# Optimization experiments

Hardware: AMD Instinct MI355X
Metric: run time of the kernel (lower is better)

## Reference

```python
import jax, jax.numpy as jnp
import numpy as np

B, S, D, E, HD, F, L, CYCLES = 2, 1024, 1000, 20, 50, 2048, 14, 3


def setup_inputs() -> dict:
    key = jax.random.key(0)
    k = jax.random.split(key, 8)
    sc = 0.02
    return {
        "x": jax.random.normal(k[0], (B, S, D), jnp.float32),
        "expert_w": jax.random.normal(k[1], (L, E, D, 3 * HD), jnp.float32) * sc,
        "expert_b": jnp.zeros((L, E, 3 * HD), jnp.float32),
        "router_w": jax.random.normal(k[2], (L, D, E), jnp.float32) * sc,
        "router_b": jnp.zeros((L, E), jnp.float32),
        "out_w": jax.random.normal(k[3], (L, D, D), jnp.float32) * sc,
        "out_b": jnp.zeros((L, D), jnp.float32),
        "ln1_g": jnp.ones((L, D), jnp.float32),
        "ln1_b": jnp.zeros((L, D), jnp.float32),
        "ff_w1": jax.random.normal(k[4], (L, D, F), jnp.float32) * sc,
        "ff_b1": jnp.zeros((L, F), jnp.float32),
        "ff_w2": jax.random.normal(k[5], (L, F, D), jnp.float32) * sc,
        "ff_b2": jnp.zeros((L, D), jnp.float32),
        "ln2_g": jnp.ones((L, D), jnp.float32),
        "ln2_b": jnp.zeros((L, D), jnp.float32),
    }


def _layer_norm(x, g, b):
    m = jnp.mean(x, -1, keepdims=True)
    v = jnp.mean((x - m) ** 2, -1, keepdims=True)
    return (x - m) * jax.lax.rsqrt(v + 1e-5) * g + b


def _moe_attn(x, ew, eb, rw, rb, ow, ob):
    # x: [b, s, d]; ew: [E, d, 3*HD]; routing softmax over experts
    b_, s_, d_ = x.shape
    routing = jax.nn.softmax(x @ rw + rb, axis=-1)           # [b, s, E]
    qkv = jnp.einsum('bsd,edh->besh', x, ew) + eb[None, :, None, :]
    q, k, v = jnp.split(qkv, 3, axis=-1)                     # each [b, E, s, HD]
    scores = jnp.einsum('besh,beth->best', q, k) * (HD ** -0.5)
    attn = jax.nn.softmax(scores, axis=-1)
    out = jnp.einsum('best,beth->besh', attn, v)             # [b, E, s, HD]
    out = out * jnp.transpose(routing, (0, 2, 1))[..., None]
    # disjoint head slices -> reshape is exactly the torch slice-add combine
    out = jnp.transpose(out, (0, 2, 1, 3)).reshape(b_, s_, d_)
    return out @ ow + ob


def _block(x, i, p):
    a = _moe_attn(x, p['expert_w'][i], p['expert_b'][i], p['router_w'][i],
                  p['router_b'][i], p['out_w'][i], p['out_b'][i])
    x = _layer_norm(x + a, p['ln1_g'][i], p['ln1_b'][i])
    h = jax.nn.gelu(x @ p['ff_w1'][i] + p['ff_b1'][i], approximate=False)
    f = h @ p['ff_w2'][i] + p['ff_b2'][i]
    return _layer_norm(x + f, p['ln2_g'][i], p['ln2_b'][i])


def _slam(x, p):
    s = x.shape[1]
    x = _block(x, 0, p)
    bounds = [(0, min(int(s * 0.45), s)),
              (max(int(s * 0.25), 0), min(int(s * 0.65), s)),
              (max(int(s * 0.45), 0), min(int(s * 0.85), s)),
              (max(int(s * 0.65), 0), s)]
    wrap = max(min(int(s * 0.05), s // 10), 1) if s > 20 else 0
    counts = np.zeros(s, np.float32)
    for st, en in bounds:
        counts[st:en] += 1.0
    if wrap:
        counts[:wrap] += 1.0
    counts = jnp.asarray(np.maximum(counts, 1.0))[None, :, None]
    for c in range(CYCLES):
        x_new = jnp.zeros_like(x)
        for j, (st, en) in enumerate(bounds):
            li = 1 + 4 * c + j
            if j == 3 and wrap:
                seg = jnp.concatenate([x[:, st:s], x[:, :wrap]], axis=1)
                out = _block(seg, li, p)
                x_new = x_new.at[:, st:s].add(out[:, :s - st])
                x_new = x_new.at[:, :wrap].add(out[:, s - st:])
            else:
                out = _block(x[:, st:en], li, p)
                x_new = x_new.at[:, st:en].add(out)
        x = x_new / counts
    return _block(x, L - 1, p)


def reference(x, expert_w, expert_b, router_w, router_b, out_w, out_b,
              ln1_g, ln1_b, ff_w1, ff_b1, ff_w2, ff_b2, ln2_g, ln2_b):
    p = dict(expert_w=expert_w, expert_b=expert_b, router_w=router_w,
             router_b=router_b, out_w=out_w, out_b=out_b, ln1_g=ln1_g,
             ln1_b=ln1_b, ff_w1=ff_w1, ff_b1=ff_b1, ff_w2=ff_w2,
             ff_b2=ff_b2, ln2_g=ln2_g, ln2_b=ln2_b)
    return _slam(x, p)
```

## Files before the change

### kernel.cpp

```cpp
#include <hip/hip_runtime.h>
#include <math.h>

namespace {

constexpr int kB  = 2;
constexpr int kS  = 1024;
constexpr int kD  = 1000;
constexpr int kE  = 20;
constexpr int kHD = 50;
constexpr int kF  = 2048;
constexpr int kQKV = 3 * kHD;

__global__ __launch_bounds__(256) void zero_kernel(float* __restrict__ p, int n) {
    int i = blockIdx.x * 256 + threadIdx.x;
    if (i < n) p[i] = 0.0f;
}

__global__ __launch_bounds__(256) void gelu_kernel(float* __restrict__ p, int n) {
    int i = blockIdx.x * 256 + threadIdx.x;
    if (i < n) {
        float x = p[i];
        p[i] = 0.5f * x * (1.0f + erff(x * 0.70710678118654752440f));
    }
}

__global__ __launch_bounds__(256) void gather_kernel(const float* __restrict__ src,
                                                     float* __restrict__ dst,
                                                     int st, int sseg) {
    int i = blockIdx.x * 256 + threadIdx.x;
    int tot = kB * sseg * kD;
    if (i >= tot) return;
    int d  = i % kD;
    int tr = i / kD;
    int r  = tr % sseg;
    int b  = tr / sseg;
    int srow = st + r;
    if (srow >= kS) srow -= kS;
    dst[i] = src[(b * kS + srow) * kD + d];
}

__global__ __launch_bounds__(256) void scatter_add_kernel(const float* __restrict__ src,
                                                          float* __restrict__ dst,
                                                          int st, int sseg) {
    int i = blockIdx.x * 256 + threadIdx.x;
    int tot = kB * sseg * kD;
    if (i >= tot) return;
    int d  = i % kD;
    int tr = i / kD;
    int r  = tr % sseg;
    int b  = tr / sseg;
    int drow = st + r;
    if (drow >= kS) drow -= kS;
    dst[(b * kS + drow) * kD + d] += src[i];
}

__global__ __launch_bounds__(256) void finalize_kernel(const float* __restrict__ xn,
                                                       float* __restrict__ cur) {
    int i = blockIdx.x * 256 + threadIdx.x;
    const int tot = kB * kS * kD;
    if (i >= tot) return;
    int r = (i / kD) % kS;
    float cnt = 0.0f;
    cnt += (r < 460) ? 1.0f : 0.0f;
    cnt += (r >= 256 && r < 665) ? 1.0f : 0.0f;
    cnt += (r >= 460 && r < 870) ? 1.0f : 0.0f;
    cnt += (r >= 665) ? 1.0f : 0.0f;
    cnt += (r < 51) ? 1.0f : 0.0f;
    cnt = fmaxf(cnt, 1.0f);
    cur[i] = xn[i] / cnt;
}

template<int BM, int BN, int TM, int TN>
__global__ __launch_bounds__(256) void gemm_tile(
    const float* __restrict__ A, const float* __restrict__ W,
    const float* __restrict__ bias, float* __restrict__ C,
    int M, int N, int K,
    long long strideW, long long strideC, long long strideBias)
{
    constexpr int BK = 16;
    constexpr int TX = BN / TN;
    constexpr int TY = BM / TM;
    static_assert(TX * TY == 256, "block must be 256 threads");
    static_assert(TM % 4 == 0 && TN % 4 == 0, "vector frags");

    W    += (long long)blockIdx.z * strideW;
    C    += (long long)blockIdx.z * strideC;
    bias += (long long)blockIdx.z * strideBias;

    __shared__ float As[BK][BM + 4];
    __shared__ float Bs[BK][BN];

    const int tid  = threadIdx.x;
    const int tx   = tid % TX;
    const int ty   = tid / TX;
    const int row0 = blockIdx.y * BM;
    const int col0 = blockIdx.x * BN;

    const bool nvec = (N % 4) == 0;
    const bool kvec = (K % 4) == 0;

    float acc[TM][TN] = {};

    const int nk = (K + BK - 1) / BK;
    for (int t = 0; t < nk; t++) {
        const int k0 = t * BK;

        #pragma unroll
        for (int i = 0; i < BM / 64; i++) {
            int f  = tid + i * 256;
            int r  = f >> 2;
            int cv = f & 3;
            int gr = row0 + r;
            int gc = k0 + cv * 4;
            float4 av = make_float4(0.f, 0.f, 0.f, 0.f);
            if (gr < M) {
                if (kvec && gc + 3 < K) {
                    av = *reinterpret_cast<const float4*>(A + (long long)gr * K + gc);
                } else {
                    float t0 = (gc + 0 < K) ? A[(long long)gr * K + gc + 0] : 0.f;
                    float t1 = (gc + 1 < K) ? A[(long long)gr * K + gc + 1] : 0.f;
                    float t2 = (gc + 2 < K) ? A[(long long)gr * K + gc + 2] : 0.f;
                    float t3 = (gc + 3 < K) ? A[(long long)gr * K + gc + 3] : 0.f;
                    av = make_float4(t0, t1, t2, t3);
                }
            }
            As[cv * 4 + 0][r] = av.x;
            As[cv * 4 + 1][r] = av.y;
            As[cv * 4 + 2][r] = av.z;
            As[cv * 4 + 3][r] = av.w;
        }

        if (nvec) {
            #pragma unroll
            for (int i = 0; i < BN / 64; i++) {
                int f  = tid + i * 256;
                int r  = f / (BN / 4);
                int cv = f % (BN / 4);
                int gr = k0 + r;
                int gc = col0 + cv * 4;
                float4 bv = make_float4(0.f, 0.f, 0.f, 0.f);
                if (gr < K) {
                    if (gc + 3 < N) {
                        bv = *reinterpret_cast<const float4*>(W + (long long)gr * N + gc);
                    } else {
                        float t0 = (gc + 0 < N) ? W[(long long)gr * N + gc + 0] : 0.f;
                        float t1 = (gc + 1 < N) ? W[(long long)gr * N + gc + 1] : 0.f;
                        float t2 = (gc + 2 < N) ? W[(long long)gr * N + gc + 2] : 0.f;
                        float t3 = (gc + 3 < N) ? W[(long long)gr * N + gc + 3] : 0.f;
                        bv = make_float4(t0, t1, t2, t3);
                    }
                }
                *reinterpret_cast<float4*>(&Bs[r][cv * 4]) = bv;
            }
        } else {
            for (int idx = tid; idx < BK * BN; idx += 256) {
                int r = idx / BN, c = idx % BN;
                int gr = k0 + r, gc = col0 + c;
                Bs[r][c] = (gr < K && gc < N) ? W[(long long)gr * N + gc] : 0.f;
            }
        }
        __syncthreads();

        #pragma unroll
        for (int kk = 0; kk < BK; kk++) {
            float a[TM], b[TN];
            #pragma unroll
            for (int i = 0; i < TM; i += 4) {
                float4 v = *reinterpret_cast<const float4*>(&As[kk][ty * TM + i]);
                a[i] = v.x; a[i + 1] = v.y; a[i + 2] = v.z; a[i + 3] = v.w;
            }
            #pragma unroll
            for (int j = 0; j < TN; j += 4) {
                float4 v = *reinterpret_cast<const float4*>(&Bs[kk][tx * TN + j]);
                b[j] = v.x; b[j + 1] = v.y; b[j + 2] = v.z; b[j + 3] = v.w;
            }
            #pragma unroll
            for (int i = 0; i < TM; i++)
                #pragma unroll
                for (int j = 0; j < TN; j++)
                    acc[i][j] = fmaf(a[i], b[j], acc[i][j]);
        }
        __syncthreads();
    }

    #pragma unroll
    for (int i = 0; i < TM; i++) {
        int gr = row0 + ty * TM + i;
        if (gr >= M) continue;
        if (nvec) {
            #pragma unroll
            for (int j = 0; j < TN; j += 4) {
                int gc = col0 + tx * TN + j;
                if (gc + 3 < N) {
                    float4 bv = *reinterpret_cast<const float4*>(bias + gc);
                    float4 o  = make_float4(acc[i][j + 0] + bv.x,
                                            acc[i][j + 1] + bv.y,
                                            acc[i][j + 2] + bv.z,
                                            acc[i][j + 3] + bv.w);
                    *reinterpret_cast<float4*>(C + (long long)gr * N + gc) = o;
                } else {
                    for (int jj = 0; jj < 4; jj++) {
                        int g = gc + jj;
                        if (g < N) C[(long long)gr * N + g] = acc[i][j + jj] + bias[g];
                    }
                }
            }
        } else {
            #pragma unroll
            for (int j = 0; j < TN; j++) {
                int gc = col0 + tx * TN + j;
                if (gc < N) C[(long long)gr * N + gc] = acc[i][j] + bias[gc];
            }
        }
    }
}

template<int BM, int BN, int TM, int TN>
inline void launch_gemm(const float* A, const float* W, const float* bias, float* C,
                        int M, int N, int K, int Z,
                        long long sW, long long sC, long long sB, hipStream_t stream)
{
    dim3 grid((N + BN - 1) / BN, (M + BM - 1) / BM, Z);
    gemm_tile<BM, BN, TM, TN><<<grid, 256, 0, stream>>>(A, W, bias, C, M, N, K, sW, sC, sB);
}

__global__ __launch_bounds__(256) void routing_kernel(
    const float* __restrict__ X, const float* __restrict__ RW,
    const float* __restrict__ RB, float* __restrict__ R, int T)
{
    int wave = (blockIdx.x * 256 + threadIdx.x) / 64;
    int lane = threadIdx.x & 63;
    if (wave >= T) return;
    const float* x = X + (long long)wave * kD;

    float xr[16];
    #pragma unroll
    for (int i = 0; i < 16; i++) {
        int d = lane + 64 * i;
        xr[i] = (d < kD) ? x[d] : 0.0f;
    }
    float r[kE];
    #pragma unroll
    for (int e = 0; e < kE; e++) {
        float acc = 0.0f;
        #pragma unroll
        for (int i = 0; i < 16; i++) {
            int d = lane + 64 * i;
            if (d < kD) acc = fmaf(xr[i], RW[d * kE + e], acc);
        }
        #pragma unroll
        for (int off = 32; off > 0; off >>= 1) acc += __shfl_xor(acc, off, 64);
        r[e] = acc + RB[e];
    }
    float m = r[0];
    #pragma unroll
    for (int e = 1; e < kE; e++) m = fmaxf(m, r[e]);
    float sum = 0.0f;
    #pragma unroll
    for (int e = 0; e < kE; e++) { r[e] = expf(r[e] - m); sum += r[e]; }
    float inv = 1.0f / sum;
    float mine = 0.0f;
    #pragma unroll
    for (int e = 0; e < kE; e++) if (lane == e) mine = r[e] * inv;
    if (lane < kE) R[(long long)wave * kE + lane] = mine;
}

__global__ __launch_bounds__(256) void attn_kernel(
    const float* __restrict__ QKV, const float* __restrict__ R,
    float* __restrict__ O, int s)
{
    const int q0 = blockIdx.x * 64;
    const int e  = blockIdx.y;
    const int b  = blockIdx.z;
    const int T  = kB * s;
    const float* base = QKV + ((long long)e * T + (long long)b * s) * kQKV;

    __shared__ float Qs[64][51];
    __shared__ float Ks[64][51];
    __shared__ float Vs[64][51];
    __shared__ float Sb[64][65];
    __shared__ float mrow[64], lrow[64], arow[64];

    const int tid = threadIdx.x;
    const int tx = tid & 15, ty = tid >> 4;

    for (int idx = tid; idx < 64 * kHD; idx += 256) {
        int r = idx / kHD, h = idx % kHD;
        int q = q0 + r;
        Qs[r][h] = (q < s) ? base[(long long)q * kQKV + h] : 0.0f;
    }
    if (tid < 64) { mrow[tid] = -1e30f; lrow[tid] = 0.0f; }

    float o[4][4] = {};

    for (int k0 = 0; k0 < s; k0 += 64) {
        const int kn = min(64, s - k0);
        __syncthreads();
        for (int idx = tid; idx < 64 * kHD; idx += 256) {
            int r = idx / kHD, h = idx % kHD;
            const float* row = base + (long long)(k0 + r) * kQKV;
            bool ok = (r < kn);
            Ks[r][h] = ok ? row[kHD + h] : 0.0f;
            Vs[r][h] = ok ? row[2 * kHD + h] : 0.0f;
        }
        __syncthreads();

        float sacc[4][4] = {};
        for (int kk = 0; kk < kHD; kk++) {
            float a[4], bb[4];
            #pragma unroll
            for (int i = 0; i < 4; i++) a[i] = Qs[ty * 4 + i][kk];
            #pragma unroll
            for (int j = 0; j < 4; j++) bb[j] = Ks[tx * 4 + j][kk];
            #pragma unroll
            for (int i = 0; i < 4; i++)
                #pragma unroll
                for (int j = 0; j < 4; j++)
                    sacc[i][j] = fmaf(a[i], bb[j], sacc[i][j]);
        }
        #pragma unroll
        for (int i = 0; i < 4; i++)
            #pragma unroll
            for (int j = 0; j < 4; j++)
                Sb[ty * 4 + i][tx * 4 + j] = sacc[i][j] * 0.14142135623730950488f;
        __syncthreads();

        if (tid < 64) {
            float m_old = mrow[tid];
            float tmax = -1e30f;
            for (int j = 0; j < kn; j++) tmax = fmaxf(tmax, Sb[tid][j]);
            float m_new = fmaxf(m_old, tmax);
            float alpha = __expf(m_old - m_new);
            float rs = 0.0f;
            for (int j = 0; j < 64; j++) {
                float p = (j < kn) ? __expf(Sb[tid][j] - m_new) : 0.0f;
                Sb[tid][j] = p;
                rs += p;
            }
            mrow[tid] = m_new;
            lrow[tid] = lrow[tid] * alpha + rs;
            arow[tid] = alpha;
        }
        __syncthreads();

        float al[4];
        #pragma unroll
        for (int i = 0; i < 4; i++) al[i] = arow[ty * 4 + i];
        #pragma unroll
        for (int i = 0; i < 4; i++)
            #pragma unroll
            for (int j = 0; j < 4; j++)
                o[i][j] *= al[i];
        for (int j = 0; j < 64; j++) {
            float p[4], v[4];
            #pragma unroll
            for (int i = 0; i < 4; i++) p[i] = Sb[ty * 4 + i][j];
            #pragma unroll
            for (int c = 0; c < 4; c++) v[c] = Vs[j][tx * 4 + c];
            #pragma unroll
            for (int i = 0; i < 4; i++)
                #pragma unroll
                for (int c = 0; c < 4; c++)
                    o[i][c] = fmaf(p[i], v[c], o[i][c]);
        }
    }

    __syncthreads();
    #pragma unroll
    for (int i = 0; i < 4; i++)
        #pragma unroll
        for (int j = 0; j < 4; j++) {
            int h = tx * 4 + j;
            if (h < kHD) Sb[ty * 4 + i][h] = o[i][j];
        }
    __syncthreads();
    for (int idx = tid; idx < 64 * kHD; idx += 256) {
        int r = idx / kHD, h = idx % kHD;
        int q = q0 + r;
        if (q < s) {
            long long t = (long long)b * s + q;
            float scale = R[t * kE + e] / lrow[r];
            O[t * kD + e * kHD + h] = Sb[r][h] * scale;
        }
    }
}

__global__ __launch_bounds__(256) void ln_kernel(
    const float* __restrict__ Xres, const float* __restrict__ A,
    const float* __restrict__ G, const float* __restrict__ Bb,
    float* __restrict__ Y)
{
    const int t = blockIdx.x;
    const float* x = Xres + (long long)t * kD;
    const float* a = A + (long long)t * kD;
    __shared__ float buf[kD];
    __shared__ float red[4];
    const int tid = threadIdx.x;

    float lsum = 0.0f;
    for (int d = tid; d < kD; d += 256) {
        float v = x[d] + a[d];
        buf[d] = v;
        lsum += v;
    }
    #pragma unroll
    for (int off = 32; off > 0; off >>= 1) lsum += __shfl_xor(lsum, off, 64);
    if ((tid & 63) == 0) red[tid >> 6] = lsum;
    __syncthreads();
    float mean = (red[0] + red[1] + red[2] + red[3]) * (1.0f / kD);

    float lv = 0.0f;
    for (int d = tid; d < kD; d += 256) {
        float u = buf[d] - mean;
        lv = fmaf(u, u, lv);
    }
    #pragma unroll
    for (int off = 32; off > 0; off >>= 1) lv += __shfl_xor(lv, off, 64);
    __syncthreads();
    if ((tid & 63) == 0) red[tid >> 6] = lv;
    __syncthreads();
    float var = (red[0] + red[1] + red[2] + red[3]) * (1.0f / kD);
    float inv = rsqrtf(var + 1e-5f);

    for (int d = tid; d < kD; d += 256)
        Y[(long long)t * kD + d] = (buf[d] - mean) * inv * G[d] + Bb[d];
}

struct Params {
    const float *expert_w, *expert_b, *router_w, *router_b, *out_w, *out_b;
    const float *ln1_g, *ln1_b, *ff_w1, *ff_b1, *ff_w2, *ff_b2, *ln2_g, *ln2_b;
};

void run_block(const float* xin, float* xout, int s, int li, const Params& P,
               float* routing, float* qkv, float* attn_comb, float* a_out,
               float* y1, float* h, float* f, hipStream_t stream)
{
    const int T = kB * s;

    routing_kernel<<<(T + 3) / 4, 256, 0, stream>>>(
        xin, P.router_w + (long long)li * kD * kE, P.router_b + li * kE, routing, T);

    launch_gemm<128, 64, 8, 4>(
        xin, P.expert_w + (long long)li * kE * kD * kQKV,
        P.expert_b + (long long)li * kE * kQKV, qkv,
        T, kQKV, kD, kE,
        (long long)kD * kQKV, (long long)T * kQKV, (long long)kQKV, stream);

    {
        dim3 grid((s + 63) / 64, kE, kB);
        attn_kernel<<<grid, 256, 0, stream>>>(qkv, routing, attn_comb, s);
    }

    if (T >= 1536)
        launch_gemm<128, 64, 8, 4>(attn_comb, P.out_w + (long long)li * kD * kD,
                                   P.out_b + li * kD, a_out, T, kD, kD, 1, 0, 0, 0, stream);
    else
        launch_gemm<64, 64, 4, 4>(attn_comb, P.out_w + (long long)li * kD * kD,
                                  P.out_b + li * kD, a_out, T, kD, kD, 1, 0, 0, 0, stream);

    ln_kernel<<<T, 256, 0, stream>>>(xin, a_out, P.ln1_g + li * kD, P.ln1_b + li * kD, y1);

    if (T >= 1536)
        launch_gemm<128, 128, 8, 8>(y1, P.ff_w1 + (long long)li * kD * kF,
                                    P.ff_b1 + li * kF, h, T, kF, kD, 1, 0, 0, 0, stream);
    else
        launch_gemm<128, 64, 8, 4>(y1, P.ff_w1 + (long long)li * kD * kF,
                                   P.ff_b1 + li * kF, h, T, kF, kD, 1, 0, 0, 0, stream);

    gelu_kernel<<<(T * kF + 255) / 256, 256, 0, stream>>>(h, T * kF);

    if (T >= 1536)
        launch_gemm<128, 64, 8, 4>(h, P.ff_w2 + (long long)li * kF * kD,
                                   P.ff_b2 + li * kD, f, T, kD, kF, 1, 0, 0, 0, stream);
    else
        launch_gemm<64, 64, 4, 4>(h, P.ff_w2 + (long long)li * kF * kD,
                                  P.ff_b2 + li * kD, f, T, kD, kF, 1, 0, 0, 0, stream);

    ln_kernel<<<T, 256, 0, stream>>>(y1, f, P.ln2_g + li * kD, P.ln2_b + li * kD, xout);
}

}

extern "C" void kernel_launch(void* const* d_in, const int* in_sizes, int n_in,
                              void* d_out, int out_size, void* d_ws, size_t ws_size,
                              hipStream_t stream)
{
    const float* x = (const float*)d_in[0];
    Params P;
    P.expert_w = (const float*)d_in[1];
    P.expert_b = (const float*)d_in[2];
    P.router_w = (const float*)d_in[3];
    P.router_b = (const float*)d_in[4];
    P.out_w    = (const float*)d_in[5];
    P.out_b    = (const float*)d_in[6];
    P.ln1_g    = (const float*)d_in[7];
    P.ln1_b    = (const float*)d_in[8];
    P.ff_w1    = (const float*)d_in[9];
    P.ff_b1    = (const float*)d_in[10];
    P.ff_w2    = (const float*)d_in[11];
    P.ff_b2    = (const float*)d_in[12];
    P.ln2_g    = (const float*)d_in[13];
    P.ln2_b    = (const float*)d_in[14];

    const int TD = kB * kS * kD;
    float* ws = (float*)d_ws;
    float* cur       = ws;  ws += TD;
    float* xnew      = ws;  ws += TD;
    float* seg       = ws;  ws += TD;
    float* routing   = ws;  ws += kB * kS * kE;
    float* qkv       = ws;  ws += kE * kB * kS * kQKV;
    float* attn_comb = ws;  ws += TD;
    float* a_out     = ws;  ws += TD;
    float* y1        = ws;  ws += TD;
    float* h         = ws;  ws += kB * kS * kF;
    float* f         = ws;  ws += TD;
    float* bout      = (float*)d_out;

    run_block(x, cur, kS, 0, P, routing, qkv, attn_comb, a_out, y1, h, f, stream);

    const int st_arr[4]  = {0, 256, 460, 665};
    const int len_arr[4] = {460, 409, 410, 410};

    for (int c = 0; c < 3; c++) {
        zero_kernel<<<(TD + 255) / 256, 256, 0, stream>>>(xnew, TD);
        for (int j = 0; j < 4; j++) {
            const int st = st_arr[j], sl = len_arr[j];
            const int li = 1 + 4 * c + j;
            const int n = kB * sl * kD;
            gather_kernel<<<(n + 255) / 256, 256, 0, stream>>>(cur, seg, st, sl);
            run_block(seg, bout, sl, li, P, routing, qkv, attn_comb, a_out, y1, h, f, stream);
            scatter_add_kernel<<<(n + 255) / 256, 256, 0, stream>>>(bout, xnew, st, sl);
        }
        finalize_kernel<<<(TD + 255) / 256, 256, 0, stream>>>(xnew, cur);
    }

    run_block(cur, (float*)d_out, kS, 13, P, routing, qkv, attn_comb, a_out, y1, h, f, stream);
}
```

Measured before the change: 12.96 ms.

## Add split-K atomic GEMM, fused expert QKV GEMM, and register-softmax attention

Introduces a split-K GEMM path that pre-fills the output with bias and accumulates partial K-chunks with atomicAdd, picking the split from the grid size so small segment GEMMs fill the GPU. The per-expert batched QKV GEMM becomes one wide GEMM over E*3*HD columns with an index map into the per-expert layout. The attention kernel moves the online softmax into registers using wave shuffles, transposes Q/K in shared memory for float4 reads, and reuses the K buffer for the probabilities. The atomics add traffic and make the sums nondeterministic, and the mapped weight loads in the QKV GEMM are scalar rather than vectorised.

```diff
diff --git a/kernel.cpp b/kernel.cpp
--- a/kernel.cpp
+++ b/kernel.cpp
@@ -22,6 +22,13 @@
         float x = p[i];
         p[i] = 0.5f * x * (1.0f + erff(x * 0.70710678118654752440f));
     }
+}
+
+__global__ __launch_bounds__(256) void init_bias_kernel(float* __restrict__ C,
+                                                        const float* __restrict__ bias,
+                                                        long long total, int N) {
+    long long i = (long long)blockIdx.x * 256 + threadIdx.x;
+    if (i < total) C[i] = bias[(int)(i % N)];
 }
 
 __global__ __launch_bounds__(256) void gather_kernel(const float* __restrict__ src,
@@ -70,11 +77,11 @@
     cur[i] = xn[i] / cnt;
 }
 
-template<int BM, int BN, int TM, int TN>
+template<int BM, int BN, int TM, int TN, int NMAP, bool ATOMIC>
 __global__ __launch_bounds__(256) void gemm_tile(
     const float* __restrict__ A, const float* __restrict__ W,
     const float* __restrict__ bias, float* __restrict__ C,
-    int M, int N, int K,
+    int M, int N, int K, int kchunk,
     long long strideW, long long strideC, long long strideBias)
 {
     constexpr int BK = 16;
@@ -83,12 +90,18 @@
     static_assert(TX * TY == 256, "block must be 256 threads");
     static_assert(TM % 4 == 0 && TN % 4 == 0, "vector frags");
 
-    W    += (long long)blockIdx.z * strideW;
-    C    += (long long)blockIdx.z * strideC;
-    bias += (long long)blockIdx.z * strideBias;
-
-    __shared__ float As[BK][BM + 4];
-    __shared__ float Bs[BK][BN];
+    int kbeg = 0, kend = K;
+    if (ATOMIC) {
+        kbeg = blockIdx.z * kchunk;
+        kend = min(K, kbeg + kchunk);
+    } else {
+        W    += (long long)blockIdx.z * strideW;
+        C    += (long long)blockIdx.z * strideC;
+        bias += (long long)blockIdx.z * strideBias;
+    }
+
+    __shared__ __align__(16) float As[BK][BM + 4];
+    __shared__ __align__(16) float Bs[BK][BN];
 
     const int tid  = threadIdx.x;
     const int tx   = tid % TX;
@@ -96,15 +109,9 @@
     const int row0 = blockIdx.y * BM;
     const int col0 = blockIdx.x * BN;
 
-    const bool nvec = (N % 4) == 0;
-    const bool kvec = (K % 4) == 0;
-
     float acc[TM][TN] = {};
 
-    const int nk = (K + BK - 1) / BK;
-    for (int t = 0; t < nk; t++) {
-        const int k0 = t * BK;
-
+    for (int k0 = kbeg; k0 < kend; k0 += BK) {
         #pragma unroll
         for (int i = 0; i < BM / 64; i++) {
             int f  = tid + i * 256;
@@ -114,13 +121,13 @@
             int gc = k0 + cv * 4;
             float4 av = make_float4(0.f, 0.f, 0.f, 0.f);
             if (gr < M) {
-                if (kvec && gc + 3 < K) {
+                if (gc + 3 < kend) {
                     av = *reinterpret_cast<const float4*>(A + (long long)gr * K + gc);
                 } else {
-                    float t0 = (gc + 0 < K) ? A[(long long)gr * K + gc + 0] : 0.f;
-                    float t1 = (gc + 1 < K) ? A[(long long)gr * K + gc + 1] : 0.f;
-                    float t2 = (gc + 2 < K) ? A[(long long)gr * K + gc + 2] : 0.f;
-                    float t3 = (gc + 3 < K) ? A[(long long)gr * K + gc + 3] : 0.f;
+                    float t0 = (gc + 0 < kend) ? A[(long long)gr * K + gc + 0] : 0.f;
+                    float t1 = (gc + 1 < kend) ? A[(long long)gr * K + gc + 1] : 0.f;
+                    float t2 = (gc + 2 < kend) ? A[(long long)gr * K + gc + 2] : 0.f;
+                    float t3 = (gc + 3 < kend) ? A[(long long)gr * K + gc + 3] : 0.f;
                     av = make_float4(t0, t1, t2, t3);
                 }
             }
@@ -130,7 +137,21 @@
             As[cv * 4 + 3][r] = av.w;
         }
 
-        if (nvec) {
+        if (NMAP > 0) {
+            #pragma unroll
+            for (int it = 0; it < (BK * BN) / 256; it++) {
+                int idx = tid + it * 256;
+                int r = idx / BN, c = idx % BN;
+                int gr = k0 + r, gc = col0 + c;
+                float v = 0.f;
+                if (gr < kend && gc < N) {
+                    int e = gc / NMAP;
+                    int n = gc - e * NMAP;
+                    v = W[(long long)e * K * NMAP + (long long)gr * NMAP + n];
+                }
+                Bs[r][c] = v;
+            }
+        } else {
             #pragma unroll
             for (int i = 0; i < BN / 64; i++) {
                 int f  = tid + i * 256;
@@ -139,7 +160,7 @@
                 int gr = k0 + r;
                 int gc = col0 + cv * 4;
                 float4 bv = make_float4(0.f, 0.f, 0.f, 0.f);
-                if (gr < K) {
+                if (gr < kend) {
                     if (gc + 3 < N) {
                         bv = *reinterpret_cast<const float4*>(W + (long long)gr * N + gc);
                     } else {
@@ -152,12 +173,6 @@
                 }
                 *reinterpret_cast<float4*>(&Bs[r][cv * 4]) = bv;
             }
-        } else {
-            for (int idx = tid; idx < BK * BN; idx += 256) {
-                int r = idx / BN, c = idx % BN;
-                int gr = k0 + r, gc = col0 + c;
-                Bs[r][c] = (gr < K && gc < N) ? W[(long long)gr * N + gc] : 0.f;
-            }
         }
         __syncthreads();
 
@@ -187,7 +202,24 @@
     for (int i = 0; i < TM; i++) {
         int gr = row0 + ty * TM + i;
         if (gr >= M) continue;
-        if (nvec) {
+        if (ATOMIC) {
+            #pragma unroll
+            for (int j = 0; j < TN; j++) {
+                int gc = col0 + tx * TN + j;
+                if (gc < N) atomicAdd(&C[(long long)gr * N + gc], acc[i][j]);
+            }
+        } else if (NMAP > 0) {
+            #pragma unroll
+            for (int j = 0; j < TN; j++) {
+                int gc = col0 + tx * TN + j;
+                if (gc < N) {
+                    int e = gc / NMAP;
+                    int n = gc - e * NMAP;
+                    C[(long long)e * M * NMAP + (long long)gr * NMAP + n] =
+                        acc[i][j] + bias[gc];
+                }
+            }
+        } else {
             #pragma unroll
             for (int j = 0; j < TN; j += 4) {
                 int gc = col0 + tx * TN + j;
@@ -205,23 +237,38 @@
                     }
                 }
             }
-        } else {
-            #pragma unroll
-            for (int j = 0; j < TN; j++) {
-                int gc = col0 + tx * TN + j;
-                if (gc < N) C[(long long)gr * N + gc] = acc[i][j] + bias[gc];
-            }
-        }
-    }
-}
-
-template<int BM, int BN, int TM, int TN>
-inline void launch_gemm(const float* A, const float* W, const float* bias, float* C,
-                        int M, int N, int K, int Z,
-                        long long sW, long long sC, long long sB, hipStream_t stream)
+        }
+    }
+}
+
+inline int pick_split(int gx, int gy, int K) {
+    int blocks = gx * gy;
+    int S = (512 + blocks - 1) / blocks;
+    if (S < 1) S = 1;
+    if (S > 4) S = 4;
+    while (S > 1 && (K + S - 1) / S < 64) S--;
+    return S;
+}
+
+inline void gemm_auto(const float* A, const float* W, const float* bias, float* C,
+                      int M, int N, int K, hipStream_t stream)
 {
-    dim3 grid((N + BN - 1) / BN, (M + BM - 1) / BM, Z);
-    gemm_tile<BM, BN, TM, TN><<<grid, 256, 0, stream>>>(A, W, bias, C, M, N, K, sW, sC, sB);
+    constexpr int BM = 128, BN = 64, TM = 8, TN = 4;
+    int gx = (N + BN - 1) / BN, gy = (M + BM - 1) / BM;
+    int S = pick_split(gx, gy, K);
+    if (S == 1) {
+        dim3 grid(gx, gy, 1);
+        gemm_tile<BM, BN, TM, TN, 0, false><<<grid, 256, 0, stream>>>(
+            A, W, bias, C, M, N, K, K, 0, 0, 0);
+    } else {
+        long long total = (long long)M * N;
+        init_bias_kernel<<<(unsigned)((total + 255) / 256), 256, 0, stream>>>(
+            C, bias, total, N);
+        int Kc = ((K + S - 1) / S + 15) & ~15;
+        dim3 grid(gx, gy, S);
+        gemm_tile<BM, BN, TM, TN, 0, true><<<grid, 256, 0, stream>>>(
+            A, W, nullptr, C, M, N, K, Kc, 0, 0, 0);
+    }
 }
 
 __global__ __launch_bounds__(256) void routing_kernel(
@@ -264,6 +311,10 @@
     for (int e = 0; e < kE; e++) if (lane == e) mine = r[e] * inv;
     if (lane < kE) R[(long long)wave * kE + lane] = mine;
 }
+
+constexpr int QT_STR = 68;
+constexpr int VS_STR = 52;
+constexpr int SB_STR = 68;
 
 __global__ __launch_bounds__(256) void attn_kernel(
     const float* __restrict__ QKV, const float* __restrict__ R,
@@ -275,112 +326,134 @@
     const int T  = kB * s;
     const float* base = QKV + ((long long)e * T + (long long)b * s) * kQKV;
 
-    __shared__ float Qs[64][51];
-    __shared__ float Ks[64][51];
-    __shared__ float Vs[64][51];
-    __shared__ float Sb[64][65];
-    __shared__ float mrow[64], lrow[64], arow[64];
+    __shared__ __align__(16) float Qt[kHD * QT_STR];
+    __shared__ __align__(16) float Vs[64 * VS_STR];
+    __shared__ __align__(16) float KS[64 * SB_STR];
 
     const int tid = threadIdx.x;
-    const int tx = tid & 15, ty = tid >> 4;
+    const int tx  = tid & 15;
+    const int ty  = tid >> 4;
+    const int row = ty * 4;
 
     for (int idx = tid; idx < 64 * kHD; idx += 256) {
         int r = idx / kHD, h = idx % kHD;
         int q = q0 + r;
-        Qs[r][h] = (q < s) ? base[(long long)q * kQKV + h] : 0.0f;
-    }
-    if (tid < 64) { mrow[tid] = -1e30f; lrow[tid] = 0.0f; }
+        Qt[h * QT_STR + r] = (q < s) ? base[(long long)q * kQKV + h] : 0.0f;
+    }
 
     float o[4][4] = {};
-
-    for (int k0 = 0; k0 < s; k0 += 64) {
+    float m[4] = {-1e30f, -1e30f, -1e30f, -1e30f};
+    float l[4] = {};
+
+    const int ntile = (s + 63) / 64;
+    for (int t = 0; t < ntile; t++) {
+        const int k0 = t * 64;
         const int kn = min(64, s - k0);
+
         __syncthreads();
         for (int idx = tid; idx < 64 * kHD; idx += 256) {
             int r = idx / kHD, h = idx % kHD;
-            const float* row = base + (long long)(k0 + r) * kQKV;
+            const float* rowp = base + (long long)(k0 + r) * kQKV;
             bool ok = (r < kn);
-            Ks[r][h] = ok ? row[kHD + h] : 0.0f;
-            Vs[r][h] = ok ? row[2 * kHD + h] : 0.0f;
+            KS[h * SB_STR + r]  = ok ? rowp[kHD + h] : 0.0f;
+            Vs[r * VS_STR + h]  = ok ? rowp[2 * kHD + h] : 0.0f;
         }
         __syncthreads();
 
         float sacc[4][4] = {};
+        #pragma unroll 2
         for (int kk = 0; kk < kHD; kk++) {
-            float a[4], bb[4];
-            #pragma unroll
-            for (int i = 0; i < 4; i++) a[i] = Qs[ty * 4 + i][kk];
-            #pragma unroll
-            for (int j = 0; j < 4; j++) bb[j] = Ks[tx * 4 + j][kk];
+            float4 a4 = *reinterpret_cast<const float4*>(&Qt[kk * QT_STR + row]);
+            float4 b4 = *reinterpret_cast<const float4*>(&KS[kk * SB_STR + tx * 4]);
+            const float av[4] = {a4.x, a4.y, a4.z, a4.w};
+            const float bv[4] = {b4.x, b4.y, b4.z, b4.w};
             #pragma unroll
             for (int i = 0; i < 4; i++)
                 #pragma unroll
                 for (int j = 0; j < 4; j++)
-                    sacc[i][j] = fmaf(a[i], bb[j], sacc[i][j]);
-        }
+                    sacc[i][j] = fmaf(av[i], bv[j], sacc[i][j]);
+        }
+
+        #pragma unroll
+        for (int i = 0; i < 4; i++) {
+            #pragma unroll
+            for (int j = 0; j < 4; j++) {
+                float v = sacc[i][j] * 0.14142135623730950488f;
+                sacc[i][j] = (tx * 4 + j < kn) ? v : -1e30f;
+            }
+            float rm = fmaxf(fmaxf(sacc[i][0], sacc[i][1]),
+                             fmaxf(sacc[i][2], sacc[i][3]));
+            rm = fmaxf(rm, __shfl_xor(rm, 1, 64));
+            rm = fmaxf(rm, __shfl_xor(rm, 2, 64));
+            rm = fmaxf(rm, __shfl_xor(rm, 4, 64));
+            rm = fmaxf(rm, __shfl_xor(rm, 8, 64));
+            float mn = fmaxf(m[i], rm);
+            float alpha = __expf(m[i] - mn);
+            m[i] = mn;
+            float rs = 0.0f;
+            #pragma unroll
+            for (int j = 0; j < 4; j++) {
+                float p = __expf(sacc[i][j] - mn);
+                sacc[i][j] = p;
+                rs += p;
+            }
+            rs += __shfl_xor(rs, 1, 64);
+            rs += __shfl_xor(rs, 2, 64);
+            rs += __shfl_xor(rs, 4, 64);
+            rs += __shfl_xor(rs, 8, 64);
+            l[i] = l[i] * alpha + rs;
+            #pragma unroll
+            for (int c = 0; c < 4; c++) o[i][c] *= alpha;
+        }
+
+        __syncthreads();
         #pragma unroll
         for (int i = 0; i < 4; i++)
-            #pragma unroll
-            for (int j = 0; j < 4; j++)
-                Sb[ty * 4 + i][tx * 4 + j] = sacc[i][j] * 0.14142135623730950488f;
+            *reinterpret_cast<float4*>(&KS[(row + i) * SB_STR + tx * 4]) =
+                make_float4(sacc[i][0], sacc[i][1], sacc[i][2], sacc[i][3]);
         __syncthreads();
 
-        if (tid < 64) {
-            float m_old = mrow[tid];
-            float tmax = -1e30f;
-            for (int j = 0; j < kn; j++) tmax = fmaxf(tmax, Sb[tid][j]);
-            float m_new = fmaxf(m_old, tmax);
-            float alpha = __expf(m_old - m_new);
-            float rs = 0.0f;
-            for (int j = 0; j < 64; j++) {
-                float p = (j < kn) ? __expf(Sb[tid][j] - m_new) : 0.0f;
-                Sb[tid][j] = p;
-                rs += p;
-            }
-            mrow[tid] = m_new;
-            lrow[tid] = lrow[tid] * alpha + rs;
-            arow[tid] = alpha;
-        }
-        __syncthreads();
-
-        float al[4];
+        #pragma unroll 2
+        for (int j0 = 0; j0 < 64; j0 += 4) {
+            float4 pr[4], vr[4];
+            #pragma unroll
+            for (int i = 0; i < 4; i++)
+                pr[i] = *reinterpret_cast<const float4*>(&KS[(row + i) * SB_STR + j0]);
+            #pragma unroll
+            for (int jj = 0; jj < 4; jj++)
+                vr[jj] = *reinterpret_cast<const float4*>(&Vs[(j0 + jj) * VS_STR + tx * 4]);
+            #pragma unroll
+            for (int i = 0; i < 4; i++) {
+                const float pv[4] = {pr[i].x, pr[i].y, pr[i].z, pr[i].w};
+                #pragma unroll
+                for (int jj = 0; jj < 4; jj++) {
+                    o[i][0] = fmaf(pv[jj], vr[jj].x, o[i][0]);
+                    o[i][1] = fmaf(pv[jj], vr[jj].y, o[i][1]);
+                    o[i][2] = fmaf(pv[jj], vr[jj].z, o[i][2]);
+                    o[i][3] = fmaf(pv[jj], vr[jj].w, o[i][3]);
+                }
+            }
+        }
+    }
+
+    const int hbase = tx * 4;
+    if (hbase < kHD) {
         #pragma unroll
-        for (int i = 0; i < 4; i++) al[i] = arow[ty * 4 + i];
-        #pragma unroll
-        for (int i = 0; i < 4; i++)
-            #pragma unroll
-            for (int j = 0; j < 4; j++)
-                o[i][j] *= al[i];
-        for (int j = 0; j < 64; j++) {
-            float p[4], v[4];
-            #pragma unroll
-            for (int i = 0; i < 4; i++) p[i] = Sb[ty * 4 + i][j];
-            #pragma unroll
-            for (int c = 0; c < 4; c++) v[c] = Vs[j][tx * 4 + c];
-            #pragma unroll
-            for (int i = 0; i < 4; i++)
-                #pragma unroll
-                for (int c = 0; c < 4; c++)
-                    o[i][c] = fmaf(p[i], v[c], o[i][c]);
-        }
-    }
-
-    __syncthreads();
-    #pragma unroll
-    for (int i = 0; i < 4; i++)
-        #pragma unroll
-        for (int j = 0; j < 4; j++) {
-            int h = tx * 4 + j;
-            if (h < kHD) Sb[ty * 4 + i][h] = o[i][j];
-        }
-    __syncthreads();
-    for (int idx = tid; idx < 64 * kHD; idx += 256) {
-        int r = idx / kHD, h = idx % kHD;
-        int q = q0 + r;
-        if (q < s) {
-            long long t = (long long)b * s + q;
-            float scale = R[t * kE + e] / lrow[r];
-            O[t * kD + e * kHD + h] = Sb[r][h] * scale;
+        for (int i = 0; i < 4; i++) {
+            int q = q0 + row + i;
+            if (q >= s) continue;
+            long long tok = (long long)b * s + q;
+            float sc = R[tok * kE + e] / l[i];
+            float* op = O + tok * kD + e * kHD + hbase;
+            if (hbase + 3 < kHD) {
+                *reinterpret_cast<float2*>(op) =
+                    make_float2(o[i][0] * sc, o[i][1] * sc);
+                *reinterpret_cast<float2*>(op + 2) =
+                    make_float2(o[i][2] * sc, o[i][3] * sc);
+            } else {
+                op[0] = o[i][0] * sc;
+                op[1] = o[i][1] * sc;
+            }
         }
     }
 }
@@ -440,41 +513,31 @@
     routing_kernel<<<(T + 3) / 4, 256, 0, stream>>>(
         xin, P.router_w + (long long)li * kD * kE, P.router_b + li * kE, routing, T);
 
-    launch_gemm<128, 64, 8, 4>(
-        xin, P.expert_w + (long long)li * kE * kD * kQKV,
-        P.expert_b + (long long)li * kE * kQKV, qkv,
-        T, kQKV, kD, kE,
-        (long long)kD * kQKV, (long long)T * kQKV, (long long)kQKV, stream);
+    {
+        dim3 grid((kE * kQKV + 63) / 64, (T + 127) / 128, 1);
+        gemm_tile<128, 64, 8, 4, kQKV, false><<<grid, 256, 0, stream>>>(
+            xin, P.expert_w + (long long)li * kE * kD * kQKV,
+            P.expert_b + (long long)li * kE * kQKV, qkv,
+            T, kE * kQKV, kD, kD, 0, 0, 0);
+    }
 
     {
         dim3 grid((s + 63) / 64, kE, kB);
         attn_kernel<<<grid, 256, 0, stream>>>(qkv, routing, attn_comb, s);
     }
 
-    if (T >= 1536)
-        launch_gemm<128, 64, 8, 4>(attn_comb, P.out_w + (long long)li * kD * kD,
-                                   P.out_b + li * kD, a_out, T, kD, kD, 1, 0, 0, 0, stream);
-    else
-        launch_gemm<64, 64, 4, 4>(attn_comb, P.out_w + (long long)li * kD * kD,
-                                  P.out_b + li * kD, a_out, T, kD, kD, 1, 0, 0, 0, stream);
+    gemm_auto(attn_comb, P.out_w + (long long)li * kD * kD,
+              P.out_b + li * kD, a_out, T, kD, kD, stream);
 
     ln_kernel<<<T, 256, 0, stream>>>(xin, a_out, P.ln1_g + li * kD, P.ln1_b + li * kD, y1);
 
-    if (T >= 1536)
-        launch_gemm<128, 128, 8, 8>(y1, P.ff_w1 + (long long)li * kD * kF,
-                                    P.ff_b1 + li * kF, h, T, kF, kD, 1, 0, 0, 0, stream);
-    else
-        launch_gemm<128, 64, 8, 4>(y1, P.ff_w1 + (long long)li * kD * kF,
-                                   P.ff_b1 + li * kF, h, T, kF, kD, 1, 0, 0, 0, stream);
+    gemm_auto(y1, P.ff_w1 + (long long)li * kD * kF,
+              P.ff_b1 + li * kF, h, T, kF, kD, stream);
 
     gelu_kernel<<<(T * kF + 255) / 256, 256, 0, stream>>>(h, T * kF);
 
-    if (T >= 1536)
-        launch_gemm<128, 64, 8, 4>(h, P.ff_w2 + (long long)li * kF * kD,
-                                   P.ff_b2 + li * kD, f, T, kD, kF, 1, 0, 0, 0, stream);
-    else
-        launch_gemm<64, 64, 4, 4>(h, P.ff_w2 + (long long)li * kF * kD,
-                                  P.ff_b2 + li * kD, f, T, kD, kF, 1, 0, 0, 0, stream);
+    gemm_auto(h, P.ff_w2 + (long long)li * kF * kD,
+              P.ff_b2 + li * kD, f, T, kD, kF, stream);
 
     ln_kernel<<<T, 256, 0, stream>>>(y1, f, P.ln2_g + li * kD, P.ln2_b + li * kD, xout);
 }
```

Result: faster. 10.56 ms (-18.5%).
